# Performance work log

Measured on AMD Instinct MI355X. Metric: run time of the kernel, lower is better.

## Reference

```python
import jax, jax.numpy as jnp
import numpy as np


def setup_inputs() -> dict:
    key = jax.random.key(0)
    kq, kk, kv = jax.random.split(key, 3)
    B, N, D = 8, 4096, 128
    Q = jax.random.normal(kq, (B, N, D), dtype=jnp.float32)
    K = jax.random.normal(kk, (B, N, D), dtype=jnp.float32)
    V = jax.random.normal(kv, (B, N, D), dtype=jnp.float32)
    return {"Q": Q, "K": K, "V": V}


def reference(Q, K, V):
    # attention = Q @ K^T  -> [B, N, N]  (scale=None, mask=None path)
    attention = jnp.einsum('bnd,bmd->bnm', Q, K)
    attention = jax.nn.softmax(attention, axis=-1)
    # context = attention @ V -> [B, N, D]
    context = jnp.einsum('bnm,bmd->bnd', attention, V)
    return context
```

## Files before the change

### kernel.cpp

```cpp
#include <hip/hip_runtime.h>

#define NB 8
#define SEQ 4096
#define DIM 128
#define BQ 128
#define KVB 64
#define NTILES (SEQ / KVB)
#define ROUNDS (NTILES / 2)
#define IMG_BYTES 32768
#define WS_NEED ((size_t)NB * NTILES * IMG_BYTES)
#define L2E 1.44269504088896f

typedef _Float16 f16x8 __attribute__((ext_vector_type(8)));
typedef __bf16 bf16x8 __attribute__((ext_vector_type(8)));
typedef float f32x4 __attribute__((ext_vector_type(4)));
typedef float f32x16 __attribute__((ext_vector_type(16)));

struct U4 { unsigned x, y, z, w; };

static __device__ __forceinline__ unsigned cvtpk_bf16(float a, float b) {
  unsigned d;
  asm("v_cvt_pk_bf16_f32 %0, %1, %2" : "=v"(d) : "v"(a), "v"(b));
  return d;
}

#define EXP2(x) __builtin_amdgcn_exp2f(x)

__global__ void prep_kv(const float* __restrict__ K, const float* __restrict__ V,
                        unsigned char* __restrict__ ws) {
  const int t = blockIdx.x;
  const int b = blockIdx.y;
  unsigned char* img = ws + ((size_t)b * NTILES + t) * IMG_BYTES;
  int4* kimg = (int4*)img;
  int4* vimg = (int4*)(img + 16384);
  const float* Kb = K + ((size_t)b * SEQ + t * KVB) * DIM;
  const float* Vb = V + ((size_t)b * SEQ + t * KVB) * DIM;
  const int tid = threadIdx.x;

#pragma unroll
  for (int p = 0; p < 4; ++p) {
    const int un = tid + 256 * p;
    const int kv = un >> 4;
    const int u = (un & 15) ^ (kv & 15);
    const int s = u >> 1, hh = u & 1;
    const float* src = Kb + (size_t)kv * DIM + 16 * s + 8 * hh;
    f16x8 hv;
#pragma unroll
    for (int j = 0; j < 8; ++j) hv[j] = (_Float16)src[j];
    kimg[un] = __builtin_bit_cast(int4, hv);
  }

#pragma unroll
  for (int p = 0; p < 4; ++p) {
    const int un = tid + 256 * p;
    const int rr = un >> 4;
    const int c = (un & 15) ^ (rr & 15);
    const int dhi = c >> 3, slot = c & 7;
    const int s2 = slot >> 1, hh = slot & 1;
    const int d = 64 * dhi + rr;
    bf16x8 hv;
#pragma unroll
    for (int e = 0; e < 8; ++e) {
      const int kv = 16 * s2 + 4 * hh + (e & 3) + 8 * (e >> 2);
      hv[e] = (__bf16)Vb[(size_t)kv * DIM + d];
    }
    vimg[un] = __builtin_bit_cast(int4, hv);
  }
}

__global__ __launch_bounds__(512, 2)
void attn_fwd10(const float* __restrict__ Q, const unsigned char* __restrict__ ws,
                float* __restrict__ O) {
  __shared__ __align__(16) unsigned char smem[131072];

  const int tid = threadIdx.x;
  const int grp = tid >> 8;
  const int w4 = (tid >> 6) & 3;
  const int l = tid & 63;
  const int l31 = l & 31;
  const int h = l >> 5;

  const int bid = blockIdx.x;
  const int b = bid & 7;
  const int qt = bid >> 3;
  const size_t base = (size_t)b * SEQ * DIM;
  const int qrow = qt * BQ + w4 * 32 + l31;

  f16x8 qf[8];
  {
    const float* qp = Q + base + (size_t)qrow * DIM + 8 * h;
#pragma unroll
    for (int s = 0; s < 8; ++s) {
      f32x4 a = *(const f32x4*)(qp + 16 * s);
      f32x4 c = *(const f32x4*)(qp + 16 * s + 4);
      f16x8 hv;
#pragma unroll
      for (int j = 0; j < 4; ++j) {
        hv[j] = (_Float16)(a[j] * L2E);
        hv[j + 4] = (_Float16)(c[j] * L2E);
      }
      qf[s] = hv;
    }
  }

  f32x16 o[4];
#pragma unroll
  for (int j = 0; j < 4; ++j) {
#pragma unroll
    for (int r = 0; r < 16; ++r) o[j][r] = 0.f;
  }
  float ls = 0.f;

  unsigned char* mybuf = smem + grp * 65536;
  const unsigned char* wsb = ws + (size_t)b * NTILES * IMG_BYTES;

  auto STAGE = [&](int t, int bufsel) {
    const unsigned char* src = wsb + (size_t)t * IMG_BYTES + w4 * 8192 + l * 16;
    unsigned char* dst = mybuf + bufsel * 32768 + w4 * 8192;
#pragma unroll
    for (int i = 0; i < 8; ++i) {
      __builtin_amdgcn_global_load_lds(
          (const __attribute__((address_space(1))) unsigned int*)(src + i * 1024),
          (__attribute__((address_space(3))) unsigned int*)(dst + i * 1024),
          16, 0, 0);
    }
  };

  const int kb2 = (l31 * 256 + ((l31 & 15) * 16)) ^ (h * 16);
  int vb[4];
#pragma unroll
  for (int j = 0; j < 4; ++j) {
    const int rr = 32 * (j & 1) + l31;
    vb[j] = 16384 + rr * 256 + ((((j >> 1) * 8 + h) ^ (rr & 15)) * 16);
  }

  STAGE(grp, 0);
  __syncthreads();

  for (int i = 0; i < ROUNDS; ++i) {
    const int cur = i & 1;
    if (i + 1 < ROUNDS) STAGE(2 * (i + 1) + grp, cur ^ 1);
    const unsigned char* bufp = mybuf + cur * 32768;

    f32x16 s0, s1;
#pragma unroll
    for (int r = 0; r < 16; ++r) { s0[r] = 0.f; s1[r] = 0.f; }
    __builtin_amdgcn_s_setprio(1);
#pragma unroll
    for (int s = 0; s < 8; ++s) {
      f16x8 k0 = *(const f16x8*)(bufp + (kb2 ^ (32 * s)));
      s0 = __builtin_amdgcn_mfma_f32_32x32x16_f16(k0, qf[s], s0, 0, 0, 0);
    }
#pragma unroll
    for (int s = 0; s < 8; ++s) {
      f16x8 k1 = *(const f16x8*)(bufp + (kb2 ^ (32 * s)) + 8192);
      s1 = __builtin_amdgcn_mfma_f32_32x32x16_f16(k1, qf[s], s1, 0, 0, 0);
    }
    __builtin_amdgcn_s_setprio(0);

    float a0 = 0.f, a1 = 0.f, a2 = 0.f, a3 = 0.f;
#pragma unroll
    for (int r = 0; r < 16; r += 4) {
      s0[r + 0] = EXP2(s0[r + 0]);
      s0[r + 1] = EXP2(s0[r + 1]);
      s0[r + 2] = EXP2(s0[r + 2]);
      s0[r + 3] = EXP2(s0[r + 3]);
      a0 += s0[r + 0]; a1 += s0[r + 1]; a2 += s0[r + 2]; a3 += s0[r + 3];
    }
    bf16x8 pb0[2];
#pragma unroll
    for (int u = 0; u < 2; ++u) {
      U4 t0 = {cvtpk_bf16(s0[8 * u + 0], s0[8 * u + 1]),
               cvtpk_bf16(s0[8 * u + 2], s0[8 * u + 3]),
               cvtpk_bf16(s0[8 * u + 4], s0[8 * u + 5]),
               cvtpk_bf16(s0[8 * u + 6], s0[8 * u + 7])};
      pb0[u] = __builtin_bit_cast(bf16x8, t0);
    }

    __builtin_amdgcn_s_setprio(1);
#pragma unroll
    for (int s2 = 0; s2 < 2; ++s2) {
#pragma unroll
      for (int j = 0; j < 4; ++j) {
        bf16x8 vf = *(const bf16x8*)(bufp + (vb[j] ^ (32 * s2)));
        o[j] = __builtin_amdgcn_mfma_f32_32x32x16_bf16(vf, pb0[s2], o[j], 0, 0, 0);
      }
    }
    __builtin_amdgcn_s_setprio(0);

#pragma unroll
    for (int r = 0; r < 16; r += 4) {
      s1[r + 0] = EXP2(s1[r + 0]);
      s1[r + 1] = EXP2(s1[r + 1]);
      s1[r + 2] = EXP2(s1[r + 2]);
      s1[r + 3] = EXP2(s1[r + 3]);
      a0 += s1[r + 0]; a1 += s1[r + 1]; a2 += s1[r + 2]; a3 += s1[r + 3];
    }
    ls += (a0 + a1) + (a2 + a3);
    bf16x8 pb1[2];
#pragma unroll
    for (int u = 0; u < 2; ++u) {
      U4 t1 = {cvtpk_bf16(s1[8 * u + 0], s1[8 * u + 1]),
               cvtpk_bf16(s1[8 * u + 2], s1[8 * u + 3]),
               cvtpk_bf16(s1[8 * u + 4], s1[8 * u + 5]),
               cvtpk_bf16(s1[8 * u + 6], s1[8 * u + 7])};
      pb1[u] = __builtin_bit_cast(bf16x8, t1);
    }

    __builtin_amdgcn_s_setprio(1);
#pragma unroll
    for (int s2 = 2; s2 < 4; ++s2) {
#pragma unroll
      for (int j = 0; j < 4; ++j) {
        bf16x8 vf = *(const bf16x8*)(bufp + (vb[j] ^ (32 * s2)));
        o[j] = __builtin_amdgcn_mfma_f32_32x32x16_bf16(vf, pb1[s2 - 2], o[j], 0, 0, 0);
      }
    }
    __builtin_amdgcn_s_setprio(0);
    __syncthreads();
  }

  ls += __shfl_xor(ls, 32);

  if (grp == 1) {
    int4* park = (int4*)(smem + w4 * 16384);
#pragma unroll
    for (int j = 0; j < 4; ++j) {
#pragma unroll
      for (int rq = 0; rq < 4; ++rq) {
        f32x4 part = {o[j][4 * rq + 0], o[j][4 * rq + 1], o[j][4 * rq + 2],
                      o[j][4 * rq + 3]};
        park[l * 16 + ((4 * j + rq) ^ (l & 7))] = __builtin_bit_cast(int4, part);
      }
    }
    if (h == 0) *(float*)(smem + 65536 + w4 * 128 + l31 * 4) = ls;
  }
  __syncthreads();

  if (grp == 0) {
    const float lsB = *(const float*)(smem + 65536 + w4 * 128 + l31 * 4);
    const float inv = 1.0f / (ls + lsB);
    const int4* park = (const int4*)(smem + w4 * 16384);
    float* Ob = O + base + (size_t)qrow * DIM;
#pragma unroll
    for (int j = 0; j < 4; ++j) {
#pragma unroll
      for (int rq = 0; rq < 4; ++rq) {
        const f32x4 ob =
            __builtin_bit_cast(f32x4, park[l * 16 + ((4 * j + rq) ^ (l & 7))]);
        f32x4 res;
#pragma unroll
        for (int r = 0; r < 4; ++r)
          res[r] = (o[j][4 * rq + r] + ob[r]) * inv;
        *(f32x4*)(Ob + 32 * j + 8 * rq + 4 * h) = res;
      }
    }
  }
}

extern "C" void kernel_launch(void* const* d_in, const int* in_sizes, int n_in,
                              void* d_out, int out_size, void* d_ws,
                              size_t ws_size, hipStream_t stream) {
  const float* Q = (const float*)d_in[0];
  const float* K = (const float*)d_in[1];
  const float* V = (const float*)d_in[2];
  float* Out = (float*)d_out;
  if (ws_size < WS_NEED) return;
  prep_kv<<<dim3(NTILES, NB), dim3(256), 0, stream>>>(K, V, (unsigned char*)d_ws);
  attn_fwd10<<<dim3(SEQ / BQ * NB), dim3(512), 0, stream>>>(
      Q, (const unsigned char*)d_ws, Out);
}
```

Baseline: 94.47 us.

## Load V fragments directly from global into registers, stage only K in LDS

```diff
diff --git a/kernel.cpp b/kernel.cpp
--- a/kernel.cpp
+++ b/kernel.cpp
@@ -41,8 +41,8 @@
   for (int p = 0; p < 4; ++p) {
     const int un = tid + 256 * p;
     const int kv = un >> 4;
-    const int u = (un & 15) ^ (kv & 15);
-    const int s = u >> 1, hh = u & 1;
+    const int c = (un & 15) ^ (kv & 15);
+    const int s = c >> 1, hh = c & 1;
     const float* src = Kb + (size_t)kv * DIM + 16 * s + 8 * hh;
     f16x8 hv;
 #pragma unroll
@@ -53,11 +53,11 @@
 #pragma unroll
   for (int p = 0; p < 4; ++p) {
     const int un = tid + 256 * p;
-    const int rr = un >> 4;
-    const int c = (un & 15) ^ (rr & 15);
-    const int dhi = c >> 3, slot = c & 7;
-    const int s2 = slot >> 1, hh = slot & 1;
-    const int d = 64 * dhi + rr;
+    const int n = un >> 6;
+    const int ll = un & 63;
+    const int s2 = n >> 2, j = n & 3;
+    const int d = 32 * j + (ll & 31);
+    const int hh = ll >> 5;
     bf16x8 hv;
 #pragma unroll
     for (int e = 0; e < 8; ++e) {
@@ -69,9 +69,9 @@
 }
 
 __global__ __launch_bounds__(512, 2)
-void attn_fwd10(const float* __restrict__ Q, const unsigned char* __restrict__ ws,
+void attn_fwd14(const float* __restrict__ Q, const unsigned char* __restrict__ ws,
                 float* __restrict__ O) {
-  __shared__ __align__(16) unsigned char smem[131072];
+  __shared__ __align__(16) unsigned char smem[66048];
 
   const int tid = threadIdx.x;
   const int grp = tid >> 8;
@@ -111,50 +111,54 @@
   }
   float ls = 0.f;
 
-  unsigned char* mybuf = smem + grp * 65536;
+  unsigned char* mybuf = smem + grp * 32768;
   const unsigned char* wsb = ws + (size_t)b * NTILES * IMG_BYTES;
 
   auto STAGE = [&](int t, int bufsel) {
-    const unsigned char* src = wsb + (size_t)t * IMG_BYTES + w4 * 8192 + l * 16;
-    unsigned char* dst = mybuf + bufsel * 32768 + w4 * 8192;
-#pragma unroll
-    for (int i = 0; i < 8; ++i) {
+    const unsigned char* src = wsb + (size_t)t * IMG_BYTES + w4 * 4096 + l * 16;
+    unsigned char* dst = mybuf + bufsel * 16384 + w4 * 4096;
+#pragma unroll
+    for (int i2 = 0; i2 < 4; ++i2) {
       __builtin_amdgcn_global_load_lds(
-          (const __attribute__((address_space(1))) unsigned int*)(src + i * 1024),
-          (__attribute__((address_space(3))) unsigned int*)(dst + i * 1024),
+          (const __attribute__((address_space(1))) unsigned int*)(src + i2 * 1024),
+          (__attribute__((address_space(3))) unsigned int*)(dst + i2 * 1024),
           16, 0, 0);
     }
   };
 
   const int kb2 = (l31 * 256 + ((l31 & 15) * 16)) ^ (h * 16);
-  int vb[4];
-#pragma unroll
-  for (int j = 0; j < 4; ++j) {
-    const int rr = 32 * (j & 1) + l31;
-    vb[j] = 16384 + rr * 256 + ((((j >> 1) * 8 + h) ^ (rr & 15)) * 16);
-  }
 
   STAGE(grp, 0);
   __syncthreads();
 
   for (int i = 0; i < ROUNDS; ++i) {
     const int cur = i & 1;
+    const unsigned char* vtile =
+        wsb + (size_t)(2 * i + grp) * IMG_BYTES + 16384 + l * 16;
+
+    bf16x8 vf0[8], vf1[8];
+#pragma unroll
+    for (int n = 0; n < 8; ++n) vf0[n] = *(const bf16x8*)(vtile + n * 1024);
+#pragma unroll
+    for (int n = 0; n < 8; ++n)
+      vf1[n] = *(const bf16x8*)(vtile + (8 + n) * 1024);
+
     if (i + 1 < ROUNDS) STAGE(2 * (i + 1) + grp, cur ^ 1);
-    const unsigned char* bufp = mybuf + cur * 32768;
+    const unsigned char* bufp = mybuf + cur * 16384;
 
     f32x16 s0, s1;
 #pragma unroll
     for (int r = 0; r < 16; ++r) { s0[r] = 0.f; s1[r] = 0.f; }
     __builtin_amdgcn_s_setprio(1);
 #pragma unroll
-    for (int s = 0; s < 8; ++s) {
-      f16x8 k0 = *(const f16x8*)(bufp + (kb2 ^ (32 * s)));
-      s0 = __builtin_amdgcn_mfma_f32_32x32x16_f16(k0, qf[s], s0, 0, 0, 0);
-    }
-#pragma unroll
-    for (int s = 0; s < 8; ++s) {
-      f16x8 k1 = *(const f16x8*)(bufp + (kb2 ^ (32 * s)) + 8192);
-      s1 = __builtin_amdgcn_mfma_f32_32x32x16_f16(k1, qf[s], s1, 0, 0, 0);
+    for (int s8 = 0; s8 < 8; ++s8) {
+      f16x8 k0 = *(const f16x8*)(bufp + (kb2 ^ (s8 << 5)));
+      s0 = __builtin_amdgcn_mfma_f32_32x32x16_f16(k0, qf[s8], s0, 0, 0, 0);
+    }
+#pragma unroll
+    for (int s8 = 0; s8 < 8; ++s8) {
+      f16x8 k1 = *(const f16x8*)(bufp + (kb2 ^ (s8 << 5)) + 8192);
+      s1 = __builtin_amdgcn_mfma_f32_32x32x16_f16(k1, qf[s8], s1, 0, 0, 0);
     }
     __builtin_amdgcn_s_setprio(0);
 
@@ -182,8 +186,8 @@
     for (int s2 = 0; s2 < 2; ++s2) {
 #pragma unroll
       for (int j = 0; j < 4; ++j) {
-        bf16x8 vf = *(const bf16x8*)(bufp + (vb[j] ^ (32 * s2)));
-        o[j] = __builtin_amdgcn_mfma_f32_32x32x16_bf16(vf, pb0[s2], o[j], 0, 0, 0);
+        o[j] = __builtin_amdgcn_mfma_f32_32x32x16_bf16(vf0[4 * s2 + j],
+                                                       pb0[s2], o[j], 0, 0, 0);
       }
     }
     __builtin_amdgcn_s_setprio(0);
@@ -209,11 +213,11 @@
 
     __builtin_amdgcn_s_setprio(1);
 #pragma unroll
-    for (int s2 = 2; s2 < 4; ++s2) {
+    for (int s2 = 0; s2 < 2; ++s2) {
 #pragma unroll
       for (int j = 0; j < 4; ++j) {
-        bf16x8 vf = *(const bf16x8*)(bufp + (vb[j] ^ (32 * s2)));
-        o[j] = __builtin_amdgcn_mfma_f32_32x32x16_bf16(vf, pb1[s2 - 2], o[j], 0, 0, 0);
+        o[j] = __builtin_amdgcn_mfma_f32_32x32x16_bf16(vf1[4 * s2 + j],
+                                                       pb1[s2], o[j], 0, 0, 0);
       }
     }
     __builtin_amdgcn_s_setprio(0);
@@ -267,6 +271,6 @@
   float* Out = (float*)d_out;
   if (ws_size < WS_NEED) return;
   prep_kv<<<dim3(NTILES, NB), dim3(256), 0, stream>>>(K, V, (unsigned char*)d_ws);
-  attn_fwd10<<<dim3(SEQ / BQ * NB), dim3(512), 0, stream>>>(
+  attn_fwd14<<<dim3(SEQ / BQ * NB), dim3(512), 0, stream>>>(
       Q, (const unsigned char*)d_ws, Out);
 }
```

Result: no change. 95.30 us (+0.9%).
